# Performance work log

Hardware: AMD Instinct MI355X
Metric: run time of the kernel (lower is better)

## Reference

```python
import jax, jax.numpy as jnp
import numpy as np

MARGIN = 0.3
NEG_FILL = 1e9  # larger than any real distance; keeps min-reduction valid


def setup_inputs() -> dict:
    key = jax.random.key(0)
    k1, k2 = jax.random.split(key)
    embeddings = jax.random.normal(k1, (4096, 256), dtype=jnp.float32)
    labels = jax.random.randint(k2, (4096,), 0, 512, dtype=jnp.int64)
    return {"embeddings": embeddings, "labels": labels}


def _pairwise_distances(embeddings):
    # Faithful to the torch version, including the zero-distance sqrt guard.
    dot = jnp.matmul(embeddings, embeddings.T)          # [B, B]
    sq = jnp.diagonal(dot)                              # [B]
    d2 = sq[None, :] - 2.0 * dot + sq[:, None]
    d2 = jnp.maximum(d2, 0.0)
    zero_mask = (d2 == 0.0).astype(embeddings.dtype)
    d = jnp.sqrt(d2 + zero_mask * 1e-16)
    return d * (1.0 - zero_mask)


def reference(embeddings, labels):
    B = labels.shape[0]
    d = _pairwise_distances(embeddings)                 # [B, B]

    same = labels[:, None] == labels[None, :]           # [B, B]
    eye = jnp.eye(B, dtype=bool)
    pos_mask = same & ~eye
    neg_mask = ~same

    has_pos = jnp.any(pos_mask, axis=1)
    has_neg = jnp.any(neg_mask, axis=1)
    valid = has_pos & has_neg                           # [B]

    # Row-wise masked reductions (distances >= 0 so -1 is a safe max fill).
    hardest_pos = jnp.max(jnp.where(pos_mask, d, -1.0), axis=1)
    hardest_neg = jnp.min(jnp.where(neg_mask, d, NEG_FILL), axis=1)

    per_anchor = jnp.maximum(hardest_pos - hardest_neg + MARGIN, 0.0)
    n_valid = jnp.sum(valid.astype(jnp.float32))
    total = jnp.sum(jnp.where(valid, per_anchor, 0.0))
    return jnp.where(n_valid > 0, total / jnp.maximum(n_valid, 1.0), 0.0)
```

## Files before the change

### kernel.cpp

```cpp
#include <hip/hip_runtime.h>
#include <hip/hip_fp16.h>

#define BN 4096
#define DIM 256
#define NBLK 32
#define NPAIR 528
#define MARGIN_F 0.3f
#define NEG_FILL_F 1e9f
#define HP_SENT_BITS 0xBF800000

typedef __attribute__((ext_vector_type(8))) _Float16 f16x8;
typedef __attribute__((ext_vector_type(4))) float f32x4;

__device__ __forceinline__ void gld_lds16(const void* g, void* l) {
    __builtin_amdgcn_global_load_lds(
        (const __attribute__((address_space(1))) unsigned int*)g,
        (__attribute__((address_space(3))) unsigned int*)l, 16, 0, 0);
}

__global__ __launch_bounds__(256) void tl_prep(const float* __restrict__ E,
                                               float* __restrict__ norms,
                                               float* __restrict__ red,
                                               ushort* __restrict__ Eh) {
    const int tid  = threadIdx.x;
    const int lane = tid & 63;
    const int row  = blockIdx.x * 4 + (tid >> 6);

    float4 v = reinterpret_cast<const float4*>(E + (size_t)row * DIM)[lane];
    float f[4] = {v.x, v.y, v.z, v.w};
    ushort hb[4];
    float s = 0.0f;
    #pragma unroll
    for (int q = 0; q < 4; ++q) {
        s += f[q] * f[q];
        hb[q] = __half_as_ushort(__float2half(f[q]));
    }
    const int kc = lane >> 1, half = lane & 1;
    const size_t co = (((size_t)(kc * BN + row)) << 3) + (size_t)(half * 4);
    *reinterpret_cast<ushort4*>(Eh + co) = make_ushort4(hb[0], hb[1], hb[2], hb[3]);

    #pragma unroll
    for (int m = 32; m; m >>= 1) s += __shfl_xor(s, m, 64);
    if (lane == 0) norms[row] = s;
    if (blockIdx.x == 0 && tid < 3) red[tid] = 0.0f;
}

__global__ __launch_bounds__(256) void tl_main(const ushort* __restrict__ Eh,
                                               const int* __restrict__ labels,
                                               const float* __restrict__ norms,
                                               float* __restrict__ pHP,
                                               float* __restrict__ pHN) {
    __shared__ __align__(16) ushort smem[2][16384];

    const int tid  = threadIdx.x;
    const int lane = tid & 63;
    const int wave = tid >> 6;
    const int wy = wave >> 1, wx = wave & 1;
    const int quad = lane >> 4, l15 = lane & 15;

    int t = blockIdx.x, ib = 0, off = 0;
    while (off + (NBLK - ib) <= t) { off += NBLK - ib; ++ib; }
    const int jb = ib + (t - off);
    const int i0 = ib * 128, j0 = jb * 128;

    f32x4 acc[4][4];
    #pragma unroll
    for (int r = 0; r < 4; ++r)
        #pragma unroll
        for (int c = 0; c < 4; ++c)
            acc[r][c] = (f32x4){0.f, 0.f, 0.f, 0.f};

    auto stage = [&](int kb, int buf) {
        #pragma unroll
        for (int s = 0; s < 8; ++s) {
            const int idx  = s * 256 + tid;
            const int part = idx >> 10;
            const int kc   = (idx >> 7) & 7;
            const int m    = idx & 127;
            const int base = part ? j0 : i0;
            const ushort* src = Eh + (((size_t)((kb * 8 + kc) * BN + base + m)) << 3);
            gld_lds16(src, &smem[buf][idx << 3]);
        }
    };

    stage(0, 0);
    #pragma unroll
    for (int kb = 0; kb < DIM / 64; ++kb) {
        const int buf = kb & 1;
        __syncthreads();
        if (kb + 1 < DIM / 64) stage(kb + 1, buf ^ 1);

        const ushort* sb = &smem[buf][0];
        #pragma unroll
        for (int h = 0; h < 2; ++h) {
            f16x8 a[4], b[4];
            #pragma unroll
            for (int r = 0; r < 4; ++r) {
                const int mi = wy * 64 + r * 16 + l15;
                a[r] = *reinterpret_cast<const f16x8*>(&sb[(((h * 4 + quad) * 128) + mi) * 8]);
            }
            #pragma unroll
            for (int c = 0; c < 4; ++c) {
                const int ni = wx * 64 + c * 16 + l15;
                b[c] = *reinterpret_cast<const f16x8*>(&sb[((1024 + (h * 4 + quad) * 128) + ni) * 8]);
            }
            #pragma unroll
            for (int c = 0; c < 4; ++c)
                #pragma unroll
                for (int r = 0; r < 4; ++r)
                    acc[r][c] = __builtin_amdgcn_mfma_f32_16x16x32_f16(a[r], b[c], acc[r][c], 0, 0, 0);
        }
    }

    const int rowBase = i0 + wy * 64;
    const int colBase = j0 + wx * 64;

    float nrow[4][4]; int lrow[4][4];
    #pragma unroll
    for (int r = 0; r < 4; ++r)
        #pragma unroll
        for (int e = 0; e < 4; ++e) {
            const int g = rowBase + r * 16 + quad * 4 + e;
            nrow[r][e] = norms[g];
            lrow[r][e] = labels[g];
        }
    float ncol[4]; int lcol[4];
    #pragma unroll
    for (int c = 0; c < 4; ++c) {
        const int g = colBase + c * 16 + l15;
        ncol[c] = norms[g];
        lcol[c] = labels[g];
    }

    float rmax[4][4], rmin[4][4], cmax[4], cmin[4];
    #pragma unroll
    for (int r = 0; r < 4; ++r)
        #pragma unroll
        for (int e = 0; e < 4; ++e) { rmax[r][e] = -1.0f; rmin[r][e] = NEG_FILL_F; }
    #pragma unroll
    for (int c = 0; c < 4; ++c) { cmax[c] = -1.0f; cmin[c] = NEG_FILL_F; }

    #pragma unroll
    for (int c = 0; c < 4; ++c) {
        const int gcol = colBase + c * 16 + l15;
        #pragma unroll
        for (int r = 0; r < 4; ++r) {
            #pragma unroll
            for (int e = 0; e < 4; ++e) {
                const int grow = rowBase + r * 16 + quad * 4 + e;
                float d2 = nrow[r][e] + ncol[c] - 2.0f * acc[r][c][e];
                d2 = fmaxf(d2, 0.0f);
                const float d = (d2 > 0.0f) ? sqrtf(d2) : 0.0f;
                if (lrow[r][e] == lcol[c]) {
                    if (grow != gcol) {
                        rmax[r][e] = fmaxf(rmax[r][e], d);
                        cmax[c]    = fmaxf(cmax[c], d);
                    }
                } else {
                    rmin[r][e] = fminf(rmin[r][e], d);
                    cmin[c]    = fminf(cmin[c], d);
                }
            }
        }
    }

    #pragma unroll
    for (int m = 1; m <= 8; m <<= 1) {
        #pragma unroll
        for (int r = 0; r < 4; ++r)
            #pragma unroll
            for (int e = 0; e < 4; ++e) {
                rmax[r][e] = fmaxf(rmax[r][e], __shfl_xor(rmax[r][e], m, 64));
                rmin[r][e] = fminf(rmin[r][e], __shfl_xor(rmin[r][e], m, 64));
            }
    }
    #pragma unroll
    for (int m = 16; m <= 32; m <<= 1) {
        #pragma unroll
        for (int c = 0; c < 4; ++c) {
            cmax[c] = fmaxf(cmax[c], __shfl_xor(cmax[c], m, 64));
            cmin[c] = fminf(cmin[c], __shfl_xor(cmin[c], m, 64));
        }
    }

    int*      srhp = reinterpret_cast<int*>(&smem[0][0]);
    unsigned* srhn = reinterpret_cast<unsigned*>(srhp + 128);
    int*      schp = srhp + 256;
    unsigned* schn = reinterpret_cast<unsigned*>(srhp + 384);
    __syncthreads();
    if (tid < 128) {
        srhp[tid] = (int)HP_SENT_BITS;
        srhn[tid] = __float_as_uint(NEG_FILL_F);
        schp[tid] = (int)HP_SENT_BITS;
        schn[tid] = __float_as_uint(NEG_FILL_F);
    }
    __syncthreads();
    if (l15 == 0) {
        #pragma unroll
        for (int r = 0; r < 4; ++r)
            #pragma unroll
            for (int e = 0; e < 4; ++e) {
                const int lr = wy * 64 + r * 16 + quad * 4 + e;
                atomicMax(&srhp[lr], __float_as_int(rmax[r][e]));
                atomicMin(&srhn[lr], __float_as_uint(rmin[r][e]));
            }
    }
    if (quad == 0) {
        #pragma unroll
        for (int c = 0; c < 4; ++c) {
            const int lc = wx * 64 + c * 16 + l15;
            atomicMax(&schp[lc], __float_as_int(cmax[c]));
            atomicMin(&schn[lc], __float_as_uint(cmin[c]));
        }
    }
    __syncthreads();
    if (tid < 128) {
        float rp = __int_as_float(srhp[tid]);
        float rn = __uint_as_float(srhn[tid]);
        const float cp = __int_as_float(schp[tid]);
        const float cn = __uint_as_float(schn[tid]);
        if (ib == jb) {
            pHP[(size_t)jb * BN + i0 + tid] = fmaxf(rp, cp);
            pHN[(size_t)jb * BN + i0 + tid] = fminf(rn, cn);
        } else {
            pHP[(size_t)jb * BN + i0 + tid] = rp;
            pHN[(size_t)jb * BN + i0 + tid] = rn;
            pHP[(size_t)ib * BN + j0 + tid] = cp;
            pHN[(size_t)ib * BN + j0 + tid] = cn;
        }
    }
}

__global__ __launch_bounds__(256) void tl_reduce(const float* __restrict__ pHP,
                                                 const float* __restrict__ pHN,
                                                 float* __restrict__ red,
                                                 float* __restrict__ out) {
    const int i = blockIdx.x * 256 + threadIdx.x;
    float hp = -1.0f, hn = NEG_FILL_F;
    #pragma unroll
    for (int s = 0; s < NBLK; ++s) {
        hp = fmaxf(hp, pHP[(size_t)s * BN + i]);
        hn = fminf(hn, pHN[(size_t)s * BN + i]);
    }
    const bool valid = (hp >= 0.0f) && (hn < NEG_FILL_F);
    const float per = fmaxf(hp - hn + MARGIN_F, 0.0f);
    float s_ = valid ? per : 0.0f;
    float c_ = valid ? 1.0f : 0.0f;
    #pragma unroll
    for (int m = 32; m; m >>= 1) {
        s_ += __shfl_xor(s_, m, 64);
        c_ += __shfl_xor(c_, m, 64);
    }
    __shared__ float as_[4], ac_[4];
    const int wid = threadIdx.x >> 6;
    if ((threadIdx.x & 63) == 0) { as_[wid] = s_; ac_[wid] = c_; }
    __syncthreads();
    if (threadIdx.x == 0) {
        const float S = as_[0] + as_[1] + as_[2] + as_[3];
        const float C = ac_[0] + ac_[1] + ac_[2] + ac_[3];
        atomicAdd(&red[0], S);
        atomicAdd(&red[1], C);
        __threadfence();
        const unsigned ticket = atomicAdd(reinterpret_cast<unsigned*>(&red[2]), 1u);
        if (ticket == gridDim.x - 1) {
            const float S2 = atomicAdd(&red[0], 0.0f);
            const float C2 = atomicAdd(&red[1], 0.0f);
            out[0] = (C2 > 0.0f) ? (S2 / fmaxf(C2, 1.0f)) : 0.0f;
        }
    }
}

extern "C" void kernel_launch(void* const* d_in, const int* in_sizes, int n_in,
                              void* d_out, int out_size, void* d_ws, size_t ws_size,
                              hipStream_t stream) {
    const float* E      = (const float*)d_in[0];
    const int*   labels = (const int*)d_in[1];

    float*  ws    = (float*)d_ws;
    float*  norms = ws;
    float*  red   = ws + 4096;
    float*  pHP   = ws + 8192;
    float*  pHN   = ws + 8192 + NBLK * BN;
    ushort* Eh    = (ushort*)(ws + 8192 + 2 * NBLK * BN);

    tl_prep<<<BN / 4, 256, 0, stream>>>(E, norms, red, Eh);
    tl_main<<<NPAIR, 256, 0, stream>>>(Eh, labels, norms, pHP, pHN);
    tl_reduce<<<BN / 256, 256, 0, stream>>>(pHP, pHN, red, (float*)d_out);
}
```

Before: 97.66 us.

## Load MFMA operands directly from global, defer sqrt to final reduce, shrink reduce blocks

The main kernel drops the LDS double-buffered staging and has each wave load its f16 A/B fragments straight from global memory into registers, with software ping-pong register buffers across the eight K steps. The epilogue runs the max/min reductions on squared distances and applies sqrt only once per row in the final reduce kernel, removing per-element sqrt. The reduce kernel uses 64-thread blocks with no LDS stage, giving more blocks and more global atomics. The cost is redundant global/L2 traffic, since each wave re-fetches operands that other waves in the block also load, and LDS sharing is lost.

```diff
diff --git a/kernel.cpp b/kernel.cpp
--- a/kernel.cpp
+++ b/kernel.cpp
@@ -12,12 +12,6 @@
 typedef __attribute__((ext_vector_type(8))) _Float16 f16x8;
 typedef __attribute__((ext_vector_type(4))) float f32x4;
 
-__device__ __forceinline__ void gld_lds16(const void* g, void* l) {
-    __builtin_amdgcn_global_load_lds(
-        (const __attribute__((address_space(1))) unsigned int*)g,
-        (__attribute__((address_space(3))) unsigned int*)l, 16, 0, 0);
-}
-
 __global__ __launch_bounds__(256) void tl_prep(const float* __restrict__ E,
                                                float* __restrict__ norms,
                                                float* __restrict__ red,
@@ -50,7 +44,7 @@
                                                const float* __restrict__ norms,
                                                float* __restrict__ pHP,
                                                float* __restrict__ pHN) {
-    __shared__ __align__(16) ushort smem[2][16384];
+    __shared__ int comb[512];
 
     const int tid  = threadIdx.x;
     const int lane = tid & 63;
@@ -70,47 +64,40 @@
         for (int c = 0; c < 4; ++c)
             acc[r][c] = (f32x4){0.f, 0.f, 0.f, 0.f};
 
-    auto stage = [&](int kb, int buf) {
-        #pragma unroll
-        for (int s = 0; s < 8; ++s) {
-            const int idx  = s * 256 + tid;
-            const int part = idx >> 10;
-            const int kc   = (idx >> 7) & 7;
-            const int m    = idx & 127;
-            const int base = part ? j0 : i0;
-            const ushort* src = Eh + (((size_t)((kb * 8 + kc) * BN + base + m)) << 3);
-            gld_lds16(src, &smem[buf][idx << 3]);
-        }
+    const ushort* baseQ = Eh + (size_t)quad * (BN * 8);
+    int rA[4], rB[4];
+    #pragma unroll
+    for (int r = 0; r < 4; ++r) rA[r] = (i0 + wy * 64 + r * 16 + l15) * 8;
+    #pragma unroll
+    for (int c = 0; c < 4; ++c) rB[c] = (j0 + wx * 64 + c * 16 + l15) * 8;
+
+    f16x8 a0[4], b0[4], a1[4], b1[4];
+    auto LD = [&](f16x8 (&A)[4], f16x8 (&B)[4], int s) {
+        const size_t so = (size_t)s * (4u * BN * 8u);
+        #pragma unroll
+        for (int r = 0; r < 4; ++r)
+            A[r] = *reinterpret_cast<const f16x8*>(baseQ + so + (size_t)rA[r]);
+        #pragma unroll
+        for (int c = 0; c < 4; ++c)
+            B[c] = *reinterpret_cast<const f16x8*>(baseQ + so + (size_t)rB[c]);
     };
-
-    stage(0, 0);
-    #pragma unroll
-    for (int kb = 0; kb < DIM / 64; ++kb) {
-        const int buf = kb & 1;
-        __syncthreads();
-        if (kb + 1 < DIM / 64) stage(kb + 1, buf ^ 1);
-
-        const ushort* sb = &smem[buf][0];
-        #pragma unroll
-        for (int h = 0; h < 2; ++h) {
-            f16x8 a[4], b[4];
-            #pragma unroll
-            for (int r = 0; r < 4; ++r) {
-                const int mi = wy * 64 + r * 16 + l15;
-                a[r] = *reinterpret_cast<const f16x8*>(&sb[(((h * 4 + quad) * 128) + mi) * 8]);
-            }
-            #pragma unroll
-            for (int c = 0; c < 4; ++c) {
-                const int ni = wx * 64 + c * 16 + l15;
-                b[c] = *reinterpret_cast<const f16x8*>(&sb[((1024 + (h * 4 + quad) * 128) + ni) * 8]);
-            }
-            #pragma unroll
-            for (int c = 0; c < 4; ++c)
-                #pragma unroll
-                for (int r = 0; r < 4; ++r)
-                    acc[r][c] = __builtin_amdgcn_mfma_f32_16x16x32_f16(a[r], b[c], acc[r][c], 0, 0, 0);
-        }
-    }
+    auto MM = [&](f16x8 (&A)[4], f16x8 (&B)[4]) {
+        #pragma unroll
+        for (int c = 0; c < 4; ++c)
+            #pragma unroll
+            for (int r = 0; r < 4; ++r)
+                acc[r][c] = __builtin_amdgcn_mfma_f32_16x16x32_f16(A[r], B[c], acc[r][c], 0, 0, 0);
+    };
+
+    LD(a0, b0, 0);
+    LD(a1, b1, 1); MM(a0, b0);
+    LD(a0, b0, 2); MM(a1, b1);
+    LD(a1, b1, 3); MM(a0, b0);
+    LD(a0, b0, 4); MM(a1, b1);
+    LD(a1, b1, 5); MM(a0, b0);
+    LD(a0, b0, 6); MM(a1, b1);
+    LD(a1, b1, 7); MM(a0, b0);
+    MM(a1, b1);
 
     const int rowBase = i0 + wy * 64;
     const int colBase = j0 + wx * 64;
@@ -150,15 +137,14 @@
                 const int grow = rowBase + r * 16 + quad * 4 + e;
                 float d2 = nrow[r][e] + ncol[c] - 2.0f * acc[r][c][e];
                 d2 = fmaxf(d2, 0.0f);
-                const float d = (d2 > 0.0f) ? sqrtf(d2) : 0.0f;
                 if (lrow[r][e] == lcol[c]) {
                     if (grow != gcol) {
-                        rmax[r][e] = fmaxf(rmax[r][e], d);
-                        cmax[c]    = fmaxf(cmax[c], d);
+                        rmax[r][e] = fmaxf(rmax[r][e], d2);
+                        cmax[c]    = fmaxf(cmax[c], d2);
                     }
                 } else {
-                    rmin[r][e] = fminf(rmin[r][e], d);
-                    cmin[c]    = fminf(cmin[c], d);
+                    rmin[r][e] = fminf(rmin[r][e], d2);
+                    cmin[c]    = fminf(cmin[c], d2);
                 }
             }
         }
@@ -183,11 +169,10 @@
         }
     }
 
-    int*      srhp = reinterpret_cast<int*>(&smem[0][0]);
-    unsigned* srhn = reinterpret_cast<unsigned*>(srhp + 128);
-    int*      schp = srhp + 256;
-    unsigned* schn = reinterpret_cast<unsigned*>(srhp + 384);
-    __syncthreads();
+    int*      srhp = comb;
+    unsigned* srhn = reinterpret_cast<unsigned*>(comb + 128);
+    int*      schp = comb + 256;
+    unsigned* schn = reinterpret_cast<unsigned*>(comb + 384);
     if (tid < 128) {
         srhp[tid] = (int)HP_SENT_BITS;
         srhn[tid] = __float_as_uint(NEG_FILL_F);
@@ -231,18 +216,20 @@
     }
 }
 
-__global__ __launch_bounds__(256) void tl_reduce(const float* __restrict__ pHP,
-                                                 const float* __restrict__ pHN,
-                                                 float* __restrict__ red,
-                                                 float* __restrict__ out) {
-    const int i = blockIdx.x * 256 + threadIdx.x;
-    float hp = -1.0f, hn = NEG_FILL_F;
+__global__ __launch_bounds__(64) void tl_reduce(const float* __restrict__ pHP,
+                                                const float* __restrict__ pHN,
+                                                float* __restrict__ red,
+                                                float* __restrict__ out) {
+    const int i = blockIdx.x * 64 + threadIdx.x;
+    float hp2 = -1.0f, hn2 = NEG_FILL_F;
     #pragma unroll
     for (int s = 0; s < NBLK; ++s) {
-        hp = fmaxf(hp, pHP[(size_t)s * BN + i]);
-        hn = fminf(hn, pHN[(size_t)s * BN + i]);
-    }
-    const bool valid = (hp >= 0.0f) && (hn < NEG_FILL_F);
+        hp2 = fmaxf(hp2, pHP[(size_t)s * BN + i]);
+        hn2 = fminf(hn2, pHN[(size_t)s * BN + i]);
+    }
+    const bool valid = (hp2 >= 0.0f) && (hn2 < NEG_FILL_F);
+    const float hp = sqrtf(fmaxf(hp2, 0.0f));
+    const float hn = sqrtf(hn2);
     const float per = fmaxf(hp - hn + MARGIN_F, 0.0f);
     float s_ = valid ? per : 0.0f;
     float c_ = valid ? 1.0f : 0.0f;
@@ -251,15 +238,9 @@
         s_ += __shfl_xor(s_, m, 64);
         c_ += __shfl_xor(c_, m, 64);
     }
-    __shared__ float as_[4], ac_[4];
-    const int wid = threadIdx.x >> 6;
-    if ((threadIdx.x & 63) == 0) { as_[wid] = s_; ac_[wid] = c_; }
-    __syncthreads();
     if (threadIdx.x == 0) {
-        const float S = as_[0] + as_[1] + as_[2] + as_[3];
-        const float C = ac_[0] + ac_[1] + ac_[2] + ac_[3];
-        atomicAdd(&red[0], S);
-        atomicAdd(&red[1], C);
+        atomicAdd(&red[0], s_);
+        atomicAdd(&red[1], c_);
         __threadfence();
         const unsigned ticket = atomicAdd(reinterpret_cast<unsigned*>(&red[2]), 1u);
         if (ticket == gridDim.x - 1) {
@@ -285,5 +266,5 @@
 
     tl_prep<<<BN / 4, 256, 0, stream>>>(E, norms, red, Eh);
     tl_main<<<NPAIR, 256, 0, stream>>>(Eh, labels, norms, pHP, pHN);
-    tl_reduce<<<BN / 256, 256, 0, stream>>>(pHP, pHN, red, (float*)d_out);
-}
+    tl_reduce<<<BN / 64, 64, 0, stream>>>(pHP, pHN, red, (float*)d_out);
+}
```

After: 92.85 us. 4.9% less time.
